# Optimization experiments

Measured on AMD Instinct MI355X. Metric: run time of the kernel, lower is better.

The kernel has to match this reference:

```python
import jax, jax.numpy as jnp
import numpy as np

DIM = 1024
NUM_HEADS = 8
HEAD_DIM = 128
MAX_SEQ_LEN = 2048
ATTN_SCALE = 0.12
RMS_EPS = 1.1920929e-07  # torch float32 eps (F.rms_norm default)


def rms_norm(x):
    return x * jax.lax.rsqrt(jnp.mean(jnp.square(x), axis=-1, keepdims=True) + RMS_EPS)


def rope_tables(T):
    # angular_freq: (1/1024)**linspace(0,1,head_dim//4), padded with head_dim//4 zeros -> length head_dim//2
    af = (1.0 / 1024.0) ** np.linspace(0.0, 1.0, HEAD_DIM // 4, dtype=np.float32)
    af = np.concatenate([af, np.zeros(HEAD_DIM // 4, dtype=np.float32)])
    t = np.arange(T, dtype=np.float32)
    theta = np.einsum('i,j->ij', t, af)  # [T, head_dim//2]
    return jnp.asarray(np.cos(theta)), jnp.asarray(np.sin(theta))


def apply_rope(x_BTHD, cos, sin):
    # cos/sin: [T, head_dim//2] -> broadcast [1,T,1,hd//2]
    c = cos[None, :, None, :]
    s = sin[None, :, None, :]
    x1, x2 = jnp.split(x_BTHD, 2, axis=-1)
    y1 = x1 * c + x2 * s
    y2 = -x1 * s + x2 * c
    return jnp.concatenate([y1, y2], axis=-1)


def setup_inputs() -> dict:
    key = jax.random.key(0)
    k1, k2, k3, k4, k5 = jax.random.split(key, 5)
    B, T = 4, 2048
    hdim = NUM_HEADS * HEAD_DIM
    std = 0.5 * DIM ** (-0.5)
    bound = (3.0 ** 0.5) * std
    x = jax.random.normal(k1, (B, T, DIM), dtype=jnp.float32)
    ve = jax.random.normal(k2, (B, T, DIM), dtype=jnp.float32)
    sa_lambdas = jax.random.uniform(k3, (2,), dtype=jnp.float32)
    qkv_w = jax.random.uniform(k4, (3, hdim, DIM), dtype=jnp.float32, minval=-bound, maxval=bound)
    # original inits c_proj to zeros; use small random so the output is non-trivial
    c_proj_weight = jax.random.normal(k5, (DIM, hdim), dtype=jnp.float32) * 0.02
    return {"x": x, "ve": ve, "sa_lambdas": sa_lambdas, "qkv_w": qkv_w,
            "c_proj_weight": c_proj_weight}


def reference(x, ve, sa_lambdas, qkv_w, c_proj_weight):
    B, T, D = x.shape
    H, hd = NUM_HEADS, HEAD_DIM
    Wqkv = qkv_w.reshape(3 * H * hd, D)
    qkv = jnp.einsum('btd,ed->bte', x, Wqkv).reshape(B, T, 3 * H, hd)
    q, k, v = jnp.split(qkv, 3, axis=-2)  # each [B,T,H,hd]
    q, k = rms_norm(q), rms_norm(k)
    cos, sin = rope_tables(T)
    q, k = apply_rope(q, cos, sin), apply_rope(k, cos, sin)
    v = sa_lambdas[0] * v + sa_lambdas[1] * ve.reshape(B, T, H, hd)
    # [B,H,T,T] scores
    attn = jnp.einsum('bqhd,bkhd->bhqk', q, k) * ATTN_SCALE
    causal = jnp.triu(jnp.ones((T, T), dtype=bool), k=1)
    attn = jnp.where(causal[None, None], -jnp.inf, attn)
    attn = jax.nn.softmax(attn, axis=-1)
    y = jnp.einsum('bhqk,bkhd->bqhd', attn, v).reshape(B, T, H * hd)
    return jnp.einsum('bte,de->btd', y, c_proj_weight)
```

## Files before the change

kernel.cpp:

```cpp
#include <hip/hip_runtime.h>

#define DIM 1024
#define NH 8
#define HD 128
#define T_SEQ 2048
#define NTOK 8192
#define QKV_N 3072
#define ATTN_SCALE 0.12f
#define RMS_EPS 1.1920929e-07f

using f32x4  = __attribute__((ext_vector_type(4))) float;
using bf16x8 = __attribute__((ext_vector_type(8))) __bf16;

__device__ __forceinline__ unsigned short f2bf(float f) {
    unsigned int u = __builtin_bit_cast(unsigned int, f);
    u += 0x7fffu + ((u >> 16) & 1u);
    return (unsigned short)(u >> 16);
}
__device__ __forceinline__ float bf2f(unsigned short s) {
    unsigned int u = ((unsigned int)s) << 16;
    return __builtin_bit_cast(float, u);
}

__device__ __forceinline__ void gll16(const void* g, void* l) {
    __builtin_amdgcn_global_load_lds(
        (const __attribute__((address_space(1))) unsigned int*)g,
        (__attribute__((address_space(3))) unsigned int*)l, 16, 0, 0);
}

#define VMCNT(n) asm volatile("s_waitcnt vmcnt(" #n ")" ::: "memory")

__global__ __launch_bounds__(256) void cvt_f32_bf16(const float* __restrict__ in,
                                                    unsigned short* __restrict__ out,
                                                    int n4) {
    int i = blockIdx.x * 256 + threadIdx.x;
    if (i < n4) {
        float4 f = ((const float4*)in)[i];
        ushort4 o;
        o.x = f2bf(f.x); o.y = f2bf(f.y); o.z = f2bf(f.z); o.w = f2bf(f.w);
        ((ushort4*)out)[i] = o;
    }
}

#define GBM 256
#define GBN 128
#define GBK 64
#define SLOT_A 32768
#define SLOT_SZ 49152

template<int OUTF32>
__global__ __launch_bounds__(512, 1) void gemm256(const unsigned short* __restrict__ A,
                                                  const unsigned short* __restrict__ B,
                                                  void* __restrict__ Cout,
                                                  int M, int N, int K, int nbn) {
    __shared__ __align__(16) char smem[147456];
    const int tid  = threadIdx.x;
    const int lane = tid & 63;
    const int w    = tid >> 6;
    const int wm   = w >> 1, wn = w & 1;
    const int lr   = lane & 15, lg = lane >> 4;
    const int xsw  = (lr & 7) << 3;

    const int chunk = gridDim.x >> 3;
    const int bid2  = (blockIdx.x & 7) * chunk + (blockIdx.x >> 3);
    const int m0 = (bid2 / nbn) * GBM;
    const int n0 = (bid2 % nbn) * GBN;

    const int rsub = lane >> 3;
    const int csw  = ((lane & 7) ^ rsub) << 3;

    char* s0 = smem;
    char* s1 = smem + SLOT_SZ;
    char* s2 = smem + 2*SLOT_SZ;

    auto stage = [&](int kt, char* slot) {
        const int kb = kt * GBK;
        #pragma unroll
        for (int i = 0; i < 4; ++i) {
            int c = w*4 + i;
            gll16(&A[(size_t)(m0 + c*8 + rsub)*K + kb + csw], slot + c*1024);
        }
        #pragma unroll
        for (int i = 0; i < 2; ++i) {
            int c = w*2 + i;
            gll16(&B[(size_t)(n0 + c*8 + rsub)*K + kb + csw], slot + SLOT_A + c*1024);
        }
    };

    f32x4 acc[4][4] = {};
    const int KT = K / GBK;

    stage(0, s0);
    stage(1, s1);
    VMCNT(6);
    __builtin_amdgcn_s_barrier();
    __builtin_amdgcn_sched_barrier(0);

    for (int t = 0; t < KT; ++t) {
        if (t + 2 < KT) stage(t + 2, s2);
        const unsigned short* sA = (const unsigned short*)s0;
        const unsigned short* sB = (const unsigned short*)(s0 + SLOT_A);
        bf16x8 bfr[4][2];
        #pragma unroll
        for (int n = 0; n < 4; ++n)
            #pragma unroll
            for (int kk = 0; kk < 2; ++kk)
                bfr[n][kk] = *(const bf16x8*)&sB[(wn*64 + n*16 + lr)*64 + ((kk*32 + lg*8) ^ xsw)];
        #pragma unroll
        for (int m = 0; m < 4; ++m) {
            bf16x8 af[2];
            #pragma unroll
            for (int kk = 0; kk < 2; ++kk)
                af[kk] = *(const bf16x8*)&sA[(wm*64 + m*16 + lr)*64 + ((kk*32 + lg*8) ^ xsw)];
            __builtin_amdgcn_s_setprio(1);
            #pragma unroll
            for (int n = 0; n < 4; ++n)
                #pragma unroll
                for (int kk = 0; kk < 2; ++kk)
                    acc[m][n] = __builtin_amdgcn_mfma_f32_16x16x32_bf16(af[kk], bfr[n][kk], acc[m][n], 0, 0, 0);
            __builtin_amdgcn_s_setprio(0);
        }
        if (t + 2 < KT) { VMCNT(6); }
        else            { VMCNT(0); }
        __builtin_amdgcn_s_barrier();
        __builtin_amdgcn_sched_barrier(0);
        char* tmp = s0; s0 = s1; s1 = s2; s2 = tmp;
    }

    __syncthreads();
    float* sc = (float*)(smem + (size_t)w * 17408);
    #pragma unroll
    for (int m = 0; m < 4; ++m)
        #pragma unroll
        for (int n = 0; n < 4; ++n)
            #pragma unroll
            for (int r = 0; r < 4; ++r)
                sc[(m*16 + lg*4 + r)*68 + n*16 + lr] = acc[m][n][r];

    if (OUTF32) {
        float* C = (float*)Cout;
        #pragma unroll
        for (int rnd = 0; rnd < 16; ++rnd) {
            int g = rnd*64 + lane;
            int row = g >> 4, c4 = (g & 15) * 4;
            float4 v = *(float4*)&sc[row*68 + c4];
            *(float4*)&C[(size_t)(m0 + wm*64 + row)*N + n0 + wn*64 + c4] = v;
        }
    } else {
        unsigned short* C = (unsigned short*)Cout;
        #pragma unroll
        for (int rnd = 0; rnd < 8; ++rnd) {
            int g = rnd*64 + lane;
            int row = g >> 3, c8 = (g & 7) * 8;
            float4 v0 = *(float4*)&sc[row*68 + c8];
            float4 v1 = *(float4*)&sc[row*68 + c8 + 4];
            uint4 o;
            o.x = f2bf(v0.x) | ((unsigned)f2bf(v0.y) << 16);
            o.y = f2bf(v0.z) | ((unsigned)f2bf(v0.w) << 16);
            o.z = f2bf(v1.x) | ((unsigned)f2bf(v1.y) << 16);
            o.w = f2bf(v1.z) | ((unsigned)f2bf(v1.w) << 16);
            *(uint4*)&C[(size_t)(m0 + wm*64 + row)*N + n0 + wn*64 + c8] = o;
        }
    }
}

__global__ __launch_bounds__(256) void qkv_post(const unsigned short* __restrict__ qkv,
                                                unsigned short* __restrict__ qO,
                                                unsigned short* __restrict__ kO) {
    int gw   = (blockIdx.x * 256 + threadIdx.x) >> 6;
    int lane = threadIdx.x & 63;
    int h     = gw & 7;
    int token = gw >> 3;
    int t     = token & (T_SEQ-1);
    int b     = token >> 11;

    const unsigned short* base = qkv + (size_t)token * QKV_N + h*HD;
    float q1 = bf2f(base[lane]),        q2 = bf2f(base[lane+64]);
    float k1 = bf2f(base[1024+lane]),   k2 = bf2f(base[1024+lane+64]);

    float sq = q1*q1 + q2*q2;
    float sk = k1*k1 + k2*k2;
    #pragma unroll
    for (int m = 1; m < 64; m <<= 1) {
        sq += __shfl_xor(sq, m);
        sk += __shfl_xor(sk, m);
    }
    float qs = rsqrtf(sq * (1.0f/128.0f) + RMS_EPS) * ATTN_SCALE;
    float ks = rsqrtf(sk * (1.0f/128.0f) + RMS_EPS);
    q1 *= qs; q2 *= qs; k1 *= ks; k2 *= ks;

    float theta = (lane < 32) ? (float)t * exp2f((float)lane * (-10.0f/31.0f)) : 0.0f;
    float sn, cs;
    sincosf(theta, &sn, &cs);
    float qy1 =  q1*cs + q2*sn, qy2 = -q1*sn + q2*cs;
    float ky1 =  k1*cs + k2*sn, ky2 = -k1*sn + k2*cs;

    size_t obase = ((size_t)(b*NH + h) * T_SEQ + t) * HD;
    qO[obase + lane]      = f2bf(qy1);
    qO[obase + lane + 64] = f2bf(qy2);
    kO[obase + lane]      = f2bf(ky1);
    kO[obase + lane + 64] = f2bf(ky2);
}

__global__ __launch_bounds__(256) void vmix_t(const unsigned short* __restrict__ qkv,
                                              const float* __restrict__ ve,
                                              const float* __restrict__ lam,
                                              unsigned short* __restrict__ vt) {
    __shared__ unsigned short lT[128*72];
    const int tid = threadIdx.x;
    const int t0  = blockIdx.x * 64;
    const int bh  = blockIdx.y;
    const int b = bh >> 3, h = bh & 7;
    const float l0 = lam[0], l1 = lam[1];

    #pragma unroll
    for (int it = 0; it < 4; ++it) {
        int g  = it*256 + tid;
        int t  = g >> 4;
        int d8 = (g & 15) << 3;
        size_t token = (size_t)b*T_SEQ + t0 + t;
        ushort4 v0 = *(const ushort4*)&qkv[token*QKV_N + 2048 + h*HD + d8];
        ushort4 v1 = *(const ushort4*)&qkv[token*QKV_N + 2048 + h*HD + d8 + 4];
        float4 e0 = *(const float4*)&ve[token*DIM + h*HD + d8];
        float4 e1 = *(const float4*)&ve[token*DIM + h*HD + d8 + 4];
        lT[(d8+0)*72 + t] = f2bf(l0*bf2f(v0.x) + l1*e0.x);
        lT[(d8+1)*72 + t] = f2bf(l0*bf2f(v0.y) + l1*e0.y);
        lT[(d8+2)*72 + t] = f2bf(l0*bf2f(v0.z) + l1*e0.z);
        lT[(d8+3)*72 + t] = f2bf(l0*bf2f(v0.w) + l1*e0.w);
        lT[(d8+4)*72 + t] = f2bf(l0*bf2f(v1.x) + l1*e1.x);
        lT[(d8+5)*72 + t] = f2bf(l0*bf2f(v1.y) + l1*e1.y);
        lT[(d8+6)*72 + t] = f2bf(l0*bf2f(v1.z) + l1*e1.z);
        lT[(d8+7)*72 + t] = f2bf(l0*bf2f(v1.w) + l1*e1.w);
    }
    __syncthreads();
    #pragma unroll
    for (int it = 0; it < 4; ++it) {
        int g  = it*256 + tid;
        int d  = g >> 3;
        int t8 = (g & 7) << 3;
        uint4 pk = *(const uint4*)&lT[d*72 + t8];
        *(uint4*)&vt[((size_t)bh*HD + d)*T_SEQ + t0 + t8] = pk;
    }
}

__global__ __launch_bounds__(256) void attn_fwd(const unsigned short* __restrict__ Q,
                                                const unsigned short* __restrict__ K,
                                                const unsigned short* __restrict__ Vt,
                                                unsigned short* __restrict__ Y) {
    __shared__ unsigned short lK[2][64*128];
    __shared__ unsigned short lV[2][128*64];
    __shared__ unsigned short lP[4][16*64];

    const int tid  = threadIdx.x;
    const int lane = tid & 63;
    const int w    = tid >> 6;
    const int lr   = lane & 15, lg = lane >> 4;

    const int lin = blockIdx.y * 16 + blockIdx.x;
    const int bh  = (lin & 7)*4 + ((lin >> 3) & 3);
    const int p   = lin >> 5;
    const int qtA = p, qtB = 31 - p;

    const unsigned short* Qg = Q  + (size_t)bh * T_SEQ * HD;
    const unsigned short* Kg = K  + (size_t)bh * T_SEQ * HD;
    const unsigned short* Vg = Vt + (size_t)bh * HD * T_SEQ;
    const int q0A = qtA*64 + w*16;
    const int q0B = qtB*64 + w*16;

    auto stage = [&](int kt, int s) {
        const int kbase = kt * 64;
        #pragma unroll
        for (int i = 0; i < 4; ++i) {
            int c = w*4 + i;
            int row = c*4 + (lane >> 4);
            int col = ((lane & 15) << 3) ^ ((row & 7) << 3);
            gll16(&Kg[(size_t)(kbase + row)*HD + col], &lK[s][c*512]);
        }
        #pragma unroll
        for (int i = 0; i < 4; ++i) {
            int c = w*4 + i;
            int row = c*8 + (lane >> 3);
            int col = ((lane & 7) << 3) ^ ((row & 7) << 3);
            gll16(&Vg[(size_t)row*T_SEQ + kbase + col], &lV[s][c*512]);
        }
    };

    bf16x8 qfA[4], qfB[4];
    #pragma unroll
    for (int kk = 0; kk < 4; ++kk) {
        qfA[kk] = *(const bf16x8*)&Qg[(size_t)(q0A + lr)*HD + kk*32 + lg*8];
        qfB[kk] = *(const bf16x8*)&Qg[(size_t)(q0B + lr)*HD + kk*32 + lg*8];
    }
    VMCNT(0);
    #pragma unroll
    for (int kk = 0; kk < 4; ++kk)
        asm volatile("" :: "v"(qfA[kk]), "v"(qfB[kk]));

    f32x4 oA[8] = {}, oB[8] = {};
    float psA[4] = {0.f,0.f,0.f,0.f}, psB[4] = {0.f,0.f,0.f,0.f};

    auto pass = [&](const bf16x8* qf, f32x4* o, float* ps, int q0, bool diag,
                    int kbase, const unsigned short* lKc, const unsigned short* lVc) {
        f32x4 sf[4];
        #pragma unroll
        for (int j = 0; j < 4; ++j) {
            f32x4 s = {0.f,0.f,0.f,0.f};
            __builtin_amdgcn_s_setprio(1);
            #pragma unroll
            for (int kk = 0; kk < 4; ++kk) {
                bf16x8 kf = *(const bf16x8*)&lKc[(j*16+lr)*128 + ((kk*32 + lg*8) ^ ((lr&7)<<3))];
                s = __builtin_amdgcn_mfma_f32_16x16x32_bf16(qf[kk], kf, s, 0, 0, 0);
            }
            __builtin_amdgcn_s_setprio(0);
            sf[j] = s;
        }
        if (diag) {
            #pragma unroll
            for (int j = 0; j < 4; ++j)
                #pragma unroll
                for (int r = 0; r < 4; ++r) {
                    int kcol = kbase + j*16 + lr;
                    int qrow = q0 + lg*4 + r;
                    if (kcol > qrow) sf[j][r] = -INFINITY;
                }
        }
        #pragma unroll
        for (int j = 0; j < 4; ++j)
            #pragma unroll
            for (int r = 0; r < 4; ++r) {
                float pp = __expf(sf[j][r]);
                sf[j][r] = pp;
                ps[r] += pp;
            }
        #pragma unroll
        for (int j = 0; j < 4; ++j)
            #pragma unroll
            for (int r = 0; r < 4; ++r) {
                int prow = lg*4 + r;
                lP[w][prow*64 + ((j*16 + lr) ^ ((prow&7)<<3))] = f2bf(sf[j][r]);
            }
        asm volatile("" ::: "memory");
        bf16x8 pf[2];
        #pragma unroll
        for (int kk = 0; kk < 2; ++kk)
            pf[kk] = *(const bf16x8*)&lP[w][lr*64 + ((kk*32 + lg*8) ^ ((lr&7)<<3))];
        #pragma unroll
        for (int n = 0; n < 8; ++n) {
            __builtin_amdgcn_s_setprio(1);
            #pragma unroll
            for (int kk = 0; kk < 2; ++kk) {
                bf16x8 vf = *(const bf16x8*)&lVc[(n*16+lr)*64 + ((kk*32 + lg*8) ^ ((lr&7)<<3))];
                o[n] = __builtin_amdgcn_mfma_f32_16x16x32_bf16(pf[kk], vf, o[n], 0, 0, 0);
            }
            __builtin_amdgcn_s_setprio(0);
        }
    };

    stage(0, 0);
    for (int kt = 0; kt <= qtB; ++kt) {
        __builtin_amdgcn_s_barrier();
        const bool pre = (kt + 1 <= qtB);
        if (pre) stage(kt + 1, (kt + 1) & 1);
        if (pre) { VMCNT(8); }
        else     { VMCNT(0); }
        __builtin_amdgcn_sched_barrier(0);
        const int kbase = kt * 64;
        const unsigned short* lKc = lK[kt & 1];
        const unsigned short* lVc = lV[kt & 1];
        if (kt <= qtA) pass(qfA, oA, psA, q0A, kt == qtA, kbase, lKc, lVc);
        pass(qfB, oB, psB, q0B, kt == qtB, kbase, lKc, lVc);
    }

    #pragma unroll
    for (int m = 1; m < 16; m <<= 1)
        #pragma unroll
        for (int r = 0; r < 4; ++r) {
            psA[r] += __shfl_xor(psA[r], m);
            psB[r] += __shfl_xor(psB[r], m);
        }
    float riA[4], riB[4];
    #pragma unroll
    for (int r = 0; r < 4; ++r) { riA[r] = 1.0f / psA[r]; riB[r] = 1.0f / psB[r]; }

    const int b = bh >> 3, h = bh & 7;
    #pragma unroll
    for (int n = 0; n < 8; ++n)
        #pragma unroll
        for (int r = 0; r < 4; ++r) {
            int d = n*16 + lr;
            int qrowA = q0A + lg*4 + r;
            int qrowB = q0B + lg*4 + r;
            Y[((size_t)(b*T_SEQ + qrowA))*DIM + h*HD + d] = f2bf(oA[n][r] * riA[r]);
            Y[((size_t)(b*T_SEQ + qrowB))*DIM + h*HD + d] = f2bf(oB[n][r] * riB[r]);
        }
}

extern "C" void kernel_launch(void* const* d_in, const int* in_sizes, int n_in,
                              void* d_out, int out_size, void* d_ws, size_t ws_size,
                              hipStream_t stream) {
    const float* x      = (const float*)d_in[0];
    const float* ve     = (const float*)d_in[1];
    const float* lam    = (const float*)d_in[2];
    const float* qkvw   = (const float*)d_in[3];
    const float* cprojw = (const float*)d_in[4];

    char* ws = (char*)d_ws;
    unsigned short* xb  = (unsigned short*)(ws);
    unsigned short* wqb = (unsigned short*)(ws + 16777216);
    unsigned short* cpb = (unsigned short*)(ws + 23068672);
    unsigned short* qkv = (unsigned short*)(ws + 25165824);
    unsigned short* qa  = (unsigned short*)(ws + 75497472);
    unsigned short* ka  = (unsigned short*)(ws + 92274688);
    unsigned short* vt  = (unsigned short*)(ws + 109051904);
    unsigned short* ya  = (unsigned short*)(ws + 125829120);

    cvt_f32_bf16<<<8192, 256, 0, stream>>>(x, xb, 2097152);
    cvt_f32_bf16<<<3072, 256, 0, stream>>>(qkvw, wqb, 786432);
    cvt_f32_bf16<<<1024, 256, 0, stream>>>(cprojw, cpb, 262144);

    gemm256<0><<<768, 512, 0, stream>>>(xb, wqb, qkv, NTOK, QKV_N, DIM, 24);
    qkv_post<<<16384, 256, 0, stream>>>(qkv, qa, ka);
    vmix_t<<<dim3(32, 32), 256, 0, stream>>>(qkv, ve, lam, vt);
    attn_fwd<<<dim3(16, 32), 256, 0, stream>>>(qa, ka, vt, ya);
    gemm256<1><<<256, 512, 0, stream>>>(ya, cpb, (float*)d_out, NTOK, DIM, DIM, 8);
}
```

Baseline: 202.1 us.

## Transpose attention score MFMA, fold log2e into Q scale, precompute RoPE table

The score MFMA now uses swapped operands, so each lane holds one query row. The softmax row sum becomes a single scalar, reduced with two shuffles and shared through LDS. The log2(e) factor is folded into the Q scale so exp2f replaces __expf, and P is packed with v_cvt_pk_bf16_f32 into a padded LDS tile without XOR swizzle. A small kernel precomputes the RoPE cos/sin table so qkv_post no longer calls sincosf, and attn_fwd gets launch_bounds(256,2). The table reuses the workspace region of xb, which is safe only because the QKV GEMM has already consumed xb.

Result: no change. 199.5 us (-1.3%).

```diff
diff --git a/kernel.cpp b/kernel.cpp
--- a/kernel.cpp
+++ b/kernel.cpp
@@ -20,6 +20,11 @@
 __device__ __forceinline__ float bf2f(unsigned short s) {
     unsigned int u = ((unsigned int)s) << 16;
     return __builtin_bit_cast(float, u);
+}
+__device__ __forceinline__ unsigned int cvtpk(float lo, float hi) {
+    unsigned int r;
+    asm("v_cvt_pk_bf16_f32 %0, %1, %2" : "=v"(r) : "v"(lo), "v"(hi));
+    return r;
 }
 
 __device__ __forceinline__ void gll16(const void* g, void* l) {
@@ -42,9 +47,15 @@
     }
 }
 
-#define GBM 256
-#define GBN 128
-#define GBK 64
+__global__ __launch_bounds__(256) void rope_tab(float2* __restrict__ tab) {
+    int idx = blockIdx.x * 256 + threadIdx.x;
+    int t = idx >> 5, i = idx & 31;
+    float th = (float)t * exp2f((float)i * (-10.0f/31.0f));
+    float sn, cs;
+    sincosf(th, &sn, &cs);
+    tab[idx] = make_float2(cs, sn);
+}
+
 #define SLOT_A 32768
 #define SLOT_SZ 49152
 
@@ -63,8 +74,8 @@
 
     const int chunk = gridDim.x >> 3;
     const int bid2  = (blockIdx.x & 7) * chunk + (blockIdx.x >> 3);
-    const int m0 = (bid2 / nbn) * GBM;
-    const int n0 = (bid2 % nbn) * GBN;
+    const int m0 = (bid2 / nbn) * 256;
+    const int n0 = (bid2 % nbn) * 128;
 
     const int rsub = lane >> 3;
     const int csw  = ((lane & 7) ^ rsub) << 3;
@@ -74,7 +85,7 @@
     char* s2 = smem + 2*SLOT_SZ;
 
     auto stage = [&](int kt, char* slot) {
-        const int kb = kt * GBK;
+        const int kb = kt * 64;
         #pragma unroll
         for (int i = 0; i < 4; ++i) {
             int c = w*4 + i;
@@ -88,7 +99,7 @@
     };
 
     f32x4 acc[4][4] = {};
-    const int KT = K / GBK;
+    const int KT = K / 64;
 
     stage(0, s0);
     stage(1, s1);
@@ -165,6 +176,7 @@
 }
 
 __global__ __launch_bounds__(256) void qkv_post(const unsigned short* __restrict__ qkv,
+                                                const float2* __restrict__ tab,
                                                 unsigned short* __restrict__ qO,
                                                 unsigned short* __restrict__ kO) {
     int gw   = (blockIdx.x * 256 + threadIdx.x) >> 6;
@@ -185,13 +197,12 @@
         sq += __shfl_xor(sq, m);
         sk += __shfl_xor(sk, m);
     }
-    float qs = rsqrtf(sq * (1.0f/128.0f) + RMS_EPS) * ATTN_SCALE;
+    float qs = rsqrtf(sq * (1.0f/128.0f) + RMS_EPS) * (ATTN_SCALE * 1.44269504088896f);
     float ks = rsqrtf(sk * (1.0f/128.0f) + RMS_EPS);
     q1 *= qs; q2 *= qs; k1 *= ks; k2 *= ks;
 
-    float theta = (lane < 32) ? (float)t * exp2f((float)lane * (-10.0f/31.0f)) : 0.0f;
-    float sn, cs;
-    sincosf(theta, &sn, &cs);
+    float cs = 1.0f, sn = 0.0f;
+    if (lane < 32) { float2 cc = tab[t*32 + lane]; cs = cc.x; sn = cc.y; }
     float qy1 =  q1*cs + q2*sn, qy2 = -q1*sn + q2*cs;
     float ky1 =  k1*cs + k2*sn, ky2 = -k1*sn + k2*cs;
 
@@ -243,13 +254,14 @@
     }
 }
 
-__global__ __launch_bounds__(256) void attn_fwd(const unsigned short* __restrict__ Q,
-                                                const unsigned short* __restrict__ K,
-                                                const unsigned short* __restrict__ Vt,
-                                                unsigned short* __restrict__ Y) {
+__global__ __launch_bounds__(256, 2) void attn_fwd(const unsigned short* __restrict__ Q,
+                                                   const unsigned short* __restrict__ K,
+                                                   const unsigned short* __restrict__ Vt,
+                                                   unsigned short* __restrict__ Y) {
     __shared__ unsigned short lK[2][64*128];
     __shared__ unsigned short lV[2][128*64];
-    __shared__ unsigned short lP[4][16*64];
+    __shared__ unsigned short lP[4][16*72];
+    __shared__ float lden[4][2][16];
 
     const int tid  = threadIdx.x;
     const int lane = tid & 63;
@@ -297,30 +309,30 @@
         asm volatile("" :: "v"(qfA[kk]), "v"(qfB[kk]));
 
     f32x4 oA[8] = {}, oB[8] = {};
-    float psA[4] = {0.f,0.f,0.f,0.f}, psB[4] = {0.f,0.f,0.f,0.f};
-
-    auto pass = [&](const bf16x8* qf, f32x4* o, float* ps, int q0, bool diag,
+    float psA = 0.f, psB = 0.f;
+
+    auto pass = [&](const bf16x8* qf, f32x4* o, float& ps, int q0, bool diag,
                     int kbase, const unsigned short* lKc, const unsigned short* lVc) {
         f32x4 sf[4];
+        __builtin_amdgcn_s_setprio(1);
         #pragma unroll
         for (int j = 0; j < 4; ++j) {
             f32x4 s = {0.f,0.f,0.f,0.f};
-            __builtin_amdgcn_s_setprio(1);
             #pragma unroll
             for (int kk = 0; kk < 4; ++kk) {
                 bf16x8 kf = *(const bf16x8*)&lKc[(j*16+lr)*128 + ((kk*32 + lg*8) ^ ((lr&7)<<3))];
-                s = __builtin_amdgcn_mfma_f32_16x16x32_bf16(qf[kk], kf, s, 0, 0, 0);
+                s = __builtin_amdgcn_mfma_f32_16x16x32_bf16(kf, qf[kk], s, 0, 0, 0);
             }
-            __builtin_amdgcn_s_setprio(0);
             sf[j] = s;
         }
+        __builtin_amdgcn_s_setprio(0);
         if (diag) {
             #pragma unroll
             for (int j = 0; j < 4; ++j)
                 #pragma unroll
                 for (int r = 0; r < 4; ++r) {
-                    int kcol = kbase + j*16 + lr;
-                    int qrow = q0 + lg*4 + r;
+                    int kcol = kbase + j*16 + lg*4 + r;
+                    int qrow = q0 + lr;
                     if (kcol > qrow) sf[j][r] = -INFINITY;
                 }
         }
@@ -328,30 +340,30 @@
         for (int j = 0; j < 4; ++j)
             #pragma unroll
             for (int r = 0; r < 4; ++r) {
-                float pp = __expf(sf[j][r]);
+                float pp = exp2f(sf[j][r]);
                 sf[j][r] = pp;
-                ps[r] += pp;
-            }
-        #pragma unroll
-        for (int j = 0; j < 4; ++j)
-            #pragma unroll
-            for (int r = 0; r < 4; ++r) {
-                int prow = lg*4 + r;
-                lP[w][prow*64 + ((j*16 + lr) ^ ((prow&7)<<3))] = f2bf(sf[j][r]);
+                ps += pp;
             }
         asm volatile("" ::: "memory");
+        #pragma unroll
+        for (int j = 0; j < 4; ++j) {
+            uint2 pk;
+            pk.x = cvtpk(sf[j][0], sf[j][1]);
+            pk.y = cvtpk(sf[j][2], sf[j][3]);
+            *(uint2*)&lP[w][lr*72 + j*16 + lg*4] = pk;
+        }
+        asm volatile("" ::: "memory");
         bf16x8 pf[2];
         #pragma unroll
         for (int kk = 0; kk < 2; ++kk)
-            pf[kk] = *(const bf16x8*)&lP[w][lr*64 + ((kk*32 + lg*8) ^ ((lr&7)<<3))];
+            pf[kk] = *(const bf16x8*)&lP[w][lr*72 + kk*32 + lg*8];
         #pragma unroll
         for (int n = 0; n < 8; ++n) {
+            bf16x8 vf0 = *(const bf16x8*)&lVc[(n*16+lr)*64 + (( 0 + lg*8) ^ ((lr&7)<<3))];
+            bf16x8 vf1 = *(const bf16x8*)&lVc[(n*16+lr)*64 + ((32 + lg*8) ^ ((lr&7)<<3))];
             __builtin_amdgcn_s_setprio(1);
-            #pragma unroll
-            for (int kk = 0; kk < 2; ++kk) {
-                bf16x8 vf = *(const bf16x8*)&lVc[(n*16+lr)*64 + ((kk*32 + lg*8) ^ ((lr&7)<<3))];
-                o[n] = __builtin_amdgcn_mfma_f32_16x16x32_bf16(pf[kk], vf, o[n], 0, 0, 0);
-            }
+            o[n] = __builtin_amdgcn_mfma_f32_16x16x32_bf16(pf[0], vf0, o[n], 0, 0, 0);
+            o[n] = __builtin_amdgcn_mfma_f32_16x16x32_bf16(pf[1], vf1, o[n], 0, 0, 0);
             __builtin_amdgcn_s_setprio(0);
         }
     };
@@ -361,8 +373,7 @@
         __builtin_amdgcn_s_barrier();
         const bool pre = (kt + 1 <= qtB);
         if (pre) stage(kt + 1, (kt + 1) & 1);
-        if (pre) { VMCNT(8); }
-        else     { VMCNT(0); }
+        if (pre) { VMCNT(8); } else { VMCNT(0); }
         __builtin_amdgcn_sched_barrier(0);
         const int kbase = kt * 64;
         const unsigned short* lKc = lK[kt & 1];
@@ -371,16 +382,16 @@
         pass(qfB, oB, psB, q0B, kt == qtB, kbase, lKc, lVc);
     }
 
-    #pragma unroll
-    for (int m = 1; m < 16; m <<= 1)
-        #pragma unroll
-        for (int r = 0; r < 4; ++r) {
-            psA[r] += __shfl_xor(psA[r], m);
-            psB[r] += __shfl_xor(psB[r], m);
-        }
+    psA += __shfl_xor(psA, 16); psA += __shfl_xor(psA, 32);
+    psB += __shfl_xor(psB, 16); psB += __shfl_xor(psB, 32);
+    if (lane < 16) { lden[w][0][lane] = psA; lden[w][1][lane] = psB; }
+    asm volatile("" ::: "memory");
     float riA[4], riB[4];
     #pragma unroll
-    for (int r = 0; r < 4; ++r) { riA[r] = 1.0f / psA[r]; riB[r] = 1.0f / psB[r]; }
+    for (int r = 0; r < 4; ++r) {
+        riA[r] = 1.0f / lden[w][0][lg*4 + r];
+        riB[r] = 1.0f / lden[w][1][lg*4 + r];
+    }
 
     const int b = bh >> 3, h = bh & 7;
     #pragma unroll
@@ -413,13 +424,15 @@
     unsigned short* ka  = (unsigned short*)(ws + 92274688);
     unsigned short* vt  = (unsigned short*)(ws + 109051904);
     unsigned short* ya  = (unsigned short*)(ws + 125829120);
+    float2* tab = (float2*)(ws);
 
     cvt_f32_bf16<<<8192, 256, 0, stream>>>(x, xb, 2097152);
     cvt_f32_bf16<<<3072, 256, 0, stream>>>(qkvw, wqb, 786432);
     cvt_f32_bf16<<<1024, 256, 0, stream>>>(cprojw, cpb, 262144);
 
     gemm256<0><<<768, 512, 0, stream>>>(xb, wqb, qkv, NTOK, QKV_N, DIM, 24);
-    qkv_post<<<16384, 256, 0, stream>>>(qkv, qa, ka);
+    rope_tab<<<256, 256, 0, stream>>>(tab);
+    qkv_post<<<16384, 256, 0, stream>>>(qkv, tab, qa, ka);
     vmix_t<<<dim3(32, 32), 256, 0, stream>>>(qkv, ve, lam, vt);
     attn_fwd<<<dim3(16, 32), 256, 0, stream>>>(qa, ka, vt, ya);
     gemm256<1><<<256, 512, 0, stream>>>(ya, cpb, (float*)d_out, NTOK, DIM, DIM, 8);
```
